# Optimization experiments

Measured on AMD Instinct MI355X. Metric: run time of the kernel, lower is better.

The kernel has to match this reference:

```python
import jax, jax.numpy as jnp
import numpy as np

N_NODES = 200000
N_EDGES = 3200000
N_GRAPHS = 64
IN_DIM, HIDDEN, OUT_DIM = 128, 16, 64


def setup_inputs() -> dict:
    key = jax.random.key(0)
    ks = jax.random.split(key, 5)
    x = jax.random.normal(ks[0], (N_NODES, IN_DIM), dtype=jnp.float32)
    edge_index = jax.random.randint(ks[1], (2, N_EDGES), 0, N_NODES, dtype=jnp.int64)
    batch = jnp.sort(jax.random.randint(ks[2], (N_NODES,), 0, N_GRAPHS, dtype=jnp.int64))
    W1 = jax.random.normal(ks[3], (IN_DIM, HIDDEN), dtype=jnp.float32) * (1.0 / np.sqrt(IN_DIM))
    W2 = jax.random.normal(ks[4], (HIDDEN, OUT_DIM), dtype=jnp.float32) * (1.0 / np.sqrt(HIDDEN))
    b1 = jnp.zeros((HIDDEN,), jnp.float32)
    b2 = jnp.zeros((OUT_DIM,), jnp.float32)
    return {"x": x, "edge_index": edge_index, "batch": batch,
            "W1": W1, "b1": b1, "W2": W2, "b2": b2, "training": 0}


def _gcn_conv(x, W, b, row, col, n_nodes):
    # PyG GCNConv: add-self-loop symmetric normalization, transform then
    # gather-from-row / scatter-add-to-col.  (row, col) already include self-loops.
    h = x @ W                                             # [N, out]
    deg = jnp.zeros((n_nodes,), h.dtype).at[col].add(1.0)  # degree incl. self-loop (>=1)
    dinv = deg ** -0.5
    norm = dinv[row] * dinv[col]                          # [E+N]
    out = jnp.zeros((n_nodes, W.shape[1]), h.dtype).at[col].add(h[row] * norm[:, None])
    return out + b


def reference(x, edge_index, batch, W1, b1, W2, b2, training):
    n = x.shape[0]
    loops = jnp.arange(n, dtype=edge_index.dtype)
    row = jnp.concatenate([edge_index[0], loops])
    col = jnp.concatenate([edge_index[1], loops])
    h = _gcn_conv(x, W1, b1, row, col, n)
    h = jax.nn.relu(h)
    # F.dropout with training=False is identity (reference is deterministic)
    h = _gcn_conv(h, W2, b2, row, col, n)
    # per-graph sum pooling: replaces the Python torch.where loop
    graph_embeds = jax.ops.segment_sum(h, batch, num_segments=N_GRAPHS)
    return graph_embeds
```

## Files before the change

kernel.cpp:

```cpp
#include <hip/hip_runtime.h>


#define TPB 256
#define CHUNK 4096
#define BK_SHIFT 9
#define NPB 512

__device__ __forceinline__ float bf2f(unsigned short u) {
    union { unsigned int i; float f; } v; v.i = ((unsigned int)u) << 16; return v.f;
}
__device__ __forceinline__ unsigned short f2bf(float f) {
    union { float f; unsigned int i; } v; v.f = f;
    unsigned int r = v.i + 0x7fff + ((v.i >> 16) & 1);
    return (unsigned short)(r >> 16);
}

__global__ __launch_bounds__(TPB) void hist_gemm_kernel(
        const int* __restrict__ col, int* __restrict__ counts,
        int E, int nblk, int nbuck,
        const float* __restrict__ x, const float* __restrict__ W1,
        unsigned short* __restrict__ h1b, int N, int nbg) {
    __shared__ int hist[NPB];
    __shared__ float w1s[128 * 16];
    int b = (int)blockIdx.x, t = threadIdx.x;
    int M = min(nblk, nbg);
    int role, id;
    if (b < 2 * M) { role = b & 1; id = b >> 1; }
    else           { role = (nblk > nbg) ? 0 : 1; id = b - M; }

    if (role == 0) {
        for (int i = t; i < nbuck; i += TPB) hist[i] = 0;
        __syncthreads();
        int e0 = id * CHUNK;
        for (int i = t; i < CHUNK; i += TPB) {
            int e = e0 + i;
            if (e < E) atomicAdd(&hist[col[e] >> BK_SHIFT], 1);
        }
        __syncthreads();
        for (int i = t; i < nbuck; i += TPB) counts[i * nblk + id] = hist[i];
        return;
    }
    for (int i = t; i < 128 * 16; i += TPB) w1s[i] = W1[i];
    __syncthreads();
    int n = id * TPB + t;
    if (n >= N) return;
    const float4* xr = (const float4*)(x + (size_t)n * 128);
    float acc[16];
#pragma unroll
    for (int k = 0; k < 16; ++k) acc[k] = 0.f;
#pragma unroll 1
    for (int g = 0; g < 8; ++g) {
        float4 v0 = xr[g * 4 + 0], v1 = xr[g * 4 + 1];
        float4 v2 = xr[g * 4 + 2], v3 = xr[g * 4 + 3];
        float xv[16] = {v0.x, v0.y, v0.z, v0.w, v1.x, v1.y, v1.z, v1.w,
                        v2.x, v2.y, v2.z, v2.w, v3.x, v3.y, v3.z, v3.w};
#pragma unroll
        for (int cc = 0; cc < 16; ++cc) {
            const float4* w4 = (const float4*)&w1s[(g * 16 + cc) * 16];
            float4 wa = w4[0], wb = w4[1], wc = w4[2], wd = w4[3];
            float xc = xv[cc];
            acc[0]  = fmaf(xc, wa.x, acc[0]);  acc[1]  = fmaf(xc, wa.y, acc[1]);
            acc[2]  = fmaf(xc, wa.z, acc[2]);  acc[3]  = fmaf(xc, wa.w, acc[3]);
            acc[4]  = fmaf(xc, wb.x, acc[4]);  acc[5]  = fmaf(xc, wb.y, acc[5]);
            acc[6]  = fmaf(xc, wb.z, acc[6]);  acc[7]  = fmaf(xc, wb.w, acc[7]);
            acc[8]  = fmaf(xc, wc.x, acc[8]);  acc[9]  = fmaf(xc, wc.y, acc[9]);
            acc[10] = fmaf(xc, wc.z, acc[10]); acc[11] = fmaf(xc, wc.w, acc[11]);
            acc[12] = fmaf(xc, wd.x, acc[12]); acc[13] = fmaf(xc, wd.y, acc[13]);
            acc[14] = fmaf(xc, wd.z, acc[14]); acc[15] = fmaf(xc, wd.w, acc[15]);
        }
    }
    unsigned int u[8];
#pragma unroll
    for (int j = 0; j < 8; ++j)
        u[j] = (unsigned int)f2bf(acc[2 * j]) | ((unsigned int)f2bf(acc[2 * j + 1]) << 16);
    uint4* o = (uint4*)(h1b + (size_t)n * 16);
    o[0] = make_uint4(u[0], u[1], u[2], u[3]);
    o[1] = make_uint4(u[4], u[5], u[6], u[7]);
}

__global__ __launch_bounds__(TPB) void scan1_kernel(const int* __restrict__ in,
                                                    int* __restrict__ out,
                                                    int* __restrict__ bsum, int L) {
    __shared__ int s[TPB];
    int t = threadIdx.x;
    int i = blockIdx.x * TPB + t;
    int d = (i < L) ? in[i] : 0;
    s[t] = d; __syncthreads();
    for (int off = 1; off < TPB; off <<= 1) {
        int v = (t >= off) ? s[t - off] : 0;
        __syncthreads();
        s[t] += v;
        __syncthreads();
    }
    if (i < L) out[i] = s[t] - d;
    if (t == TPB - 1) bsum[blockIdx.x] = s[t];
}

__global__ __launch_bounds__(1024) void scan2_kernel(int* __restrict__ bsum, int nb) {
    __shared__ int s[1024];
    int t = threadIdx.x;
    int i0 = t * 2, i1 = t * 2 + 1;
    int v0 = (i0 < nb) ? bsum[i0] : 0;
    int v1 = (i1 < nb) ? bsum[i1] : 0;
    int pv = v0 + v1;
    s[t] = pv; __syncthreads();
    for (int off = 1; off < 1024; off <<= 1) {
        int u = (t >= off) ? s[t - off] : 0;
        __syncthreads();
        s[t] += u;
        __syncthreads();
    }
    int exc = s[t] - pv;
    if (i0 < nb) bsum[i0] = exc;
    if (i1 < nb) bsum[i1] = exc + v0;
}

__device__ __forceinline__ int cbase_at(const int* counts, const int* bsum, int f) {
    return counts[f] + bsum[f >> 8];
}

__global__ __launch_bounds__(TPB) void scatter_kernel(
        const int* __restrict__ row, const int* __restrict__ col,
        const int* __restrict__ counts, const int* __restrict__ bsum,
        int E, int nblk, int nbuck, int* __restrict__ bucketed) {
    __shared__ int cur[NPB];
    int id = (int)blockIdx.x, t = threadIdx.x;
    for (int i = t; i < nbuck; i += TPB)
        cur[i] = cbase_at(counts, bsum, i * nblk + id);
    __syncthreads();
    int e0 = id * CHUNK;
    for (int i = t; i < CHUNK; i += TPB) {
        int e = e0 + i;
        if (e < E) {
            int c = col[e];
            int pos = atomicAdd(&cur[c >> BK_SHIFT], 1);
            bucketed[pos] = ((c & (NPB - 1)) << 18) | row[e];
        }
    }
}

__global__ __launch_bounds__(TPB) void sort_kernel(
        const int* __restrict__ bucketed,
        const int* __restrict__ counts, const int* __restrict__ bsum,
        int E, int nblk, int nbuck,
        int* __restrict__ csr, int* __restrict__ offs, float* __restrict__ dinv,
        const unsigned short* __restrict__ h1b, unsigned short* __restrict__ h1p, int N) {
    __shared__ int lhist[NPB];
    __shared__ int part[TPB];
    __shared__ float sdinv[NPB];
    int bk = blockIdx.x, t = threadIdx.x;
    int n0 = bk << BK_SHIFT;
    int n1 = min(n0 + NPB, N);
    int e0 = cbase_at(counts, bsum, bk * nblk);
    int e1 = (bk + 1 < nbuck) ? cbase_at(counts, bsum, (bk + 1) * nblk) : E;

    lhist[t] = 0; lhist[t + TPB] = 0;
    __syncthreads();
    for (int i = e0 + t; i < e1; i += TPB)
        atomicAdd(&lhist[bucketed[i] >> 18], 1);
    __syncthreads();

    int base = t * 2;
    int c0 = lhist[base], c1 = lhist[base + 1];
    int s = c0 + c1;
    part[t] = s;
    __syncthreads();
    for (int off = 1; off < TPB; off <<= 1) {
        int v = (t >= off) ? part[t - off] : 0;
        __syncthreads();
        part[t] += v;
        __syncthreads();
    }
    int o0 = e0 + part[t] - s;
    int o1 = o0 + c0;
    lhist[base] = o0; lhist[base + 1] = o1;
    sdinv[base]     = rsqrtf((float)c0 + 1.0f);
    sdinv[base + 1] = rsqrtf((float)c1 + 1.0f);
    int n = n0 + base;
    if (n + 0 < N) { offs[n + 0] = o0; dinv[n + 0] = sdinv[base]; }
    if (n + 1 < N) { offs[n + 1] = o1; dinv[n + 1] = sdinv[base + 1]; }
    __syncthreads();

    for (int i = e0 + t; i < e1; i += TPB) {
        int v = bucketed[i];
        int pos = atomicAdd(&lhist[v >> 18], 1);
        csr[pos] = v & 0x3FFFF;
    }
    int nq = (n1 - n0) * 4;
    for (int i = t; i < nq; i += TPB) {
        float dv = sdinv[i >> 2];
        uint2 u = ((const uint2*)h1b)[(size_t)n0 * 4 + i];
        float f0 = bf2f((unsigned short)(u.x & 0xffff));
        float f1 = bf2f((unsigned short)(u.x >> 16));
        float f2 = bf2f((unsigned short)(u.y & 0xffff));
        float f3 = bf2f((unsigned short)(u.y >> 16));
        ((ushort4*)h1p)[(size_t)n0 * 4 + i] =
            make_ushort4(f2bf(f0 * dv), f2bf(f1 * dv), f2bf(f2 * dv), f2bf(f3 * dv));
    }
    if (bk == 0 && t == 0) offs[N] = E;
}

__global__ __launch_bounds__(TPB) void gather1_kernel(const int* __restrict__ csr,
                                                      const int* __restrict__ offs,
                                                      const unsigned short* __restrict__ h1p,
                                                      const float* __restrict__ dinv,
                                                      const float* __restrict__ b1,
                                                      unsigned short* __restrict__ h2p, int N) {
    int t = threadIdx.x;
    int c = blockIdx.x * 16 + (t >> 4);
    int lane = t & 15;
    int half = lane >> 3;
    int kk = lane & 7;
    if (c >= N) return;
    int p0 = offs[c], p1 = offs[c + 1];
    float a0 = 0.f, a1 = 0.f;
    for (int p = p0; p < p1; p += 32) {
        int s_lo = csr[min(p + lane, p1 - 1)];
        int s_hi = csr[min(p + 16 + lane, p1 - 1)];
        int rem = p1 - p;
        unsigned int u[16];
#pragma unroll
        for (int j = 0; j < 8; ++j) {
            int sj = __shfl(s_lo, 2 * j + half, 16);
            u[j] = *(const unsigned int*)&h1p[(size_t)sj * 16 + 2 * kk];
        }
#pragma unroll
        for (int j = 8; j < 16; ++j) {
            int sj = __shfl(s_hi, 2 * j + half - 16, 16);
            u[j] = *(const unsigned int*)&h1p[(size_t)sj * 16 + 2 * kk];
        }
#pragma unroll
        for (int j = 0; j < 16; ++j) {
            bool ok = (2 * j + half) < rem;
            a0 += ok ? bf2f((unsigned short)(u[j] & 0xffff)) : 0.f;
            a1 += ok ? bf2f((unsigned short)(u[j] >> 16)) : 0.f;
        }
    }
    a0 += __shfl_xor(a0, 8, 16);
    a1 += __shfl_xor(a1, 8, 16);
    if (half == 0) {
        float dc = dinv[c];
        unsigned int us = *(const unsigned int*)&h1p[(size_t)c * 16 + 2 * kk];
        float s0 = bf2f((unsigned short)(us & 0xffff));
        float s1 = bf2f((unsigned short)(us >> 16));
        float r0 = fmaf(dc, a0 + s0, b1[2 * kk]);
        float r1 = fmaf(dc, a1 + s1, b1[2 * kk + 1]);
        r0 = dc * fmaxf(r0, 0.f);
        r1 = dc * fmaxf(r1, 0.f);
        unsigned int w = (unsigned int)f2bf(r0) | ((unsigned int)f2bf(r1) << 16);
        *(unsigned int*)&h2p[(size_t)c * 16 + 2 * kk] = w;
    }
}

__global__ __launch_bounds__(TPB) void gather2f_kernel(
        const int* __restrict__ csr, const int* __restrict__ offs,
        const unsigned short* __restrict__ h2p, const float* __restrict__ dinv,
        const float* __restrict__ W2, const float* __restrict__ b2,
        const int* __restrict__ batch, float* __restrict__ out, int N) {
    __shared__ float w2s[16 * 64];
    __shared__ float asT[64 * 17];
    __shared__ float pool[64];
    int t = threadIdx.x;
    for (int i = t; i < 16 * 64; i += TPB) w2s[i] = W2[i];
    if (t < 64) pool[t] = 0.f;

    int n0 = blockIdx.x * 64;
    int nLast = min(n0 + 63, N - 1);
    int g0 = batch[n0];
    bool uniform = (batch[nLast] == g0);

    int grp = t >> 4, lane = t & 15;
    int half = lane >> 3, kk = lane & 7;
#pragma unroll 1
    for (int it = 0; it < 4; ++it) {
        int m = grp * 4 + it;
        int c = n0 + m;
        if (c < N) {
            int p0 = offs[c], p1 = offs[c + 1];
            float a0 = 0.f, a1 = 0.f;
            for (int p = p0; p < p1; p += 32) {
                int s_lo = csr[min(p + lane, p1 - 1)];
                int s_hi = csr[min(p + 16 + lane, p1 - 1)];
                int rem = p1 - p;
                unsigned int u[16];
#pragma unroll
                for (int j = 0; j < 8; ++j) {
                    int sj = __shfl(s_lo, 2 * j + half, 16);
                    u[j] = *(const unsigned int*)&h2p[(size_t)sj * 16 + 2 * kk];
                }
#pragma unroll
                for (int j = 8; j < 16; ++j) {
                    int sj = __shfl(s_hi, 2 * j + half - 16, 16);
                    u[j] = *(const unsigned int*)&h2p[(size_t)sj * 16 + 2 * kk];
                }
#pragma unroll
                for (int j = 0; j < 16; ++j) {
                    bool ok = (2 * j + half) < rem;
                    a0 += ok ? bf2f((unsigned short)(u[j] & 0xffff)) : 0.f;
                    a1 += ok ? bf2f((unsigned short)(u[j] >> 16)) : 0.f;
                }
            }
            a0 += __shfl_xor(a0, 8, 16);
            a1 += __shfl_xor(a1, 8, 16);
            if (half == 0) {
                float dc = dinv[c];
                unsigned int us = *(const unsigned int*)&h2p[(size_t)c * 16 + 2 * kk];
                float s0 = bf2f((unsigned short)(us & 0xffff));
                float s1 = bf2f((unsigned short)(us >> 16));
                asT[m * 17 + 2 * kk]     = dc * (a0 + s0);
                asT[m * 17 + 2 * kk + 1] = dc * (a1 + s1);
            }
        }
    }
    __syncthreads();

    int wave = t >> 6, j = t & 63;
    float w2reg[16];
#pragma unroll
    for (int kx = 0; kx < 16; ++kx) w2reg[kx] = w2s[kx * 64 + j];
    float b2j = b2[j];
    float val = 0.f;
    int g_cur = -1;
#pragma unroll 1
    for (int mi = 0; mi < 16; ++mi) {
        int m = wave * 16 + mi;
        int c = n0 + m;
        if (c >= N) break;
        const float* ar = &asT[m * 17];
        float y = b2j;
#pragma unroll
        for (int kx = 0; kx < 16; ++kx) y = fmaf(ar[kx], w2reg[kx], y);
        if (uniform) {
            val += y;
        } else {
            int g = batch[c];
            if (g != g_cur) {
                if (g_cur >= 0) atomicAdd(&out[(size_t)g_cur * 64 + j], val);
                val = 0.f;
                g_cur = g;
            }
            val += y;
        }
    }
    if (uniform) {
        atomicAdd(&pool[j], val);
        __syncthreads();
        if (t < 64) atomicAdd(&out[(size_t)g0 * 64 + t], pool[t]);
    } else {
        if (g_cur >= 0) atomicAdd(&out[(size_t)g_cur * 64 + j], val);
    }
}

static inline size_t align64(size_t v) { return (v + 63) & ~(size_t)63; }

extern "C" void kernel_launch(void* const* d_in, const int* in_sizes, int n_in,
                              void* d_out, int out_size, void* d_ws, size_t ws_size,
                              hipStream_t stream) {
    const float* x     = (const float*)d_in[0];
    const int*   ei    = (const int*)d_in[1];
    const int*   batch = (const int*)d_in[2];
    const float* W1    = (const float*)d_in[3];
    const float* b1    = (const float*)d_in[4];
    const float* W2    = (const float*)d_in[5];
    const float* b2    = (const float*)d_in[6];

    const int N = in_sizes[0] / 128;
    const int E = in_sizes[1] / 2;
    const int* row = ei;
    const int* col = ei + E;

    const int NBLK  = (E + CHUNK - 1) / CHUNK;
    const int NBUCK = (N + NPB - 1) / NPB;
    const int L     = NBUCK * NBLK;
    const int NBS   = (L + TPB - 1) / TPB;
    const int NBG   = (N + TPB - 1) / TPB;

    char* p = (char*)d_ws;
    int*            counts   = (int*)p;            p += align64((size_t)L * 4);
    int*            bsum     = (int*)p;            p += align64(2048 * 4);
    int*            bucketed = (int*)p;            p += align64((size_t)E * 4);
    int*            csr      = (int*)p;            p += align64((size_t)E * 4);
    int*            offs     = (int*)p;            p += align64((size_t)(N + 1) * 4);
    float*          dinv     = (float*)p;          p += align64((size_t)N * 4);
    unsigned short* h1b      = (unsigned short*)p; p += align64((size_t)N * 16 * 2);
    unsigned short* h1p      = (unsigned short*)p; p += align64((size_t)N * 16 * 2);
    unsigned short* h2p      = (unsigned short*)p; p += align64((size_t)N * 16 * 2);
    float*          out      = (float*)d_out;

    hipMemsetAsync(out, 0, (size_t)out_size * sizeof(float), stream);

    hist_gemm_kernel<<<NBLK + NBG, TPB, 0, stream>>>(col, counts, E, NBLK, NBUCK,
                                                     x, W1, h1b, N, NBG);
    scan1_kernel<<<NBS, TPB, 0, stream>>>(counts, counts, bsum, L);
    scan2_kernel<<<1, 1024, 0, stream>>>(bsum, NBS);
    scatter_kernel<<<NBLK, TPB, 0, stream>>>(row, col, counts, bsum,
                                             E, NBLK, NBUCK, bucketed);
    sort_kernel<<<NBUCK, TPB, 0, stream>>>(bucketed, counts, bsum, E, NBLK, NBUCK,
                                           csr, offs, dinv, h1b, h1p, N);
    gather1_kernel<<<(N + 15) / 16, TPB, 0, stream>>>(csr, offs, h1p, dinv, b1, h2p, N);
    gather2f_kernel<<<(N + 63) / 64, TPB, 0, stream>>>(csr, offs, h2p, dinv,
                                                       W2, b2, batch, out, N);
}
```

Baseline: 378.5 us.

## Split the x@W1 GEMM across hist, scan1 and scatter kernels

The node-feature GEMM blocks (x@W1 to bf16), which used to run entirely inside the histogram kernel, are now spread over three launches: up to 128 blocks with the histogram, up to 128 with the first scan pass, and the rest with the scatter kernel. This puts the bandwidth-heavy GEMM alongside the small, latency-bound scan and the atomic-heavy scatter, so their idle hardware does GEMM work. Scan1 and scatter now need larger shared-memory footprints, which may lower occupancy. The scatter launch also grows by most of the GEMM blocks.

```diff
diff --git a/kernel.cpp b/kernel.cpp
--- a/kernel.cpp
+++ b/kernel.cpp
@@ -15,34 +15,19 @@
     return (unsigned short)(r >> 16);
 }
 
-__global__ __launch_bounds__(TPB) void hist_gemm_kernel(
-        const int* __restrict__ col, int* __restrict__ counts,
-        int E, int nblk, int nbuck,
-        const float* __restrict__ x, const float* __restrict__ W1,
-        unsigned short* __restrict__ h1b, int N, int nbg) {
-    __shared__ int hist[NPB];
-    __shared__ float w1s[128 * 16];
-    int b = (int)blockIdx.x, t = threadIdx.x;
-    int M = min(nblk, nbg);
-    int role, id;
-    if (b < 2 * M) { role = b & 1; id = b >> 1; }
-    else           { role = (nblk > nbg) ? 0 : 1; id = b - M; }
-
-    if (role == 0) {
-        for (int i = t; i < nbuck; i += TPB) hist[i] = 0;
-        __syncthreads();
-        int e0 = id * CHUNK;
-        for (int i = t; i < CHUNK; i += TPB) {
-            int e = e0 + i;
-            if (e < E) atomicAdd(&hist[col[e] >> BK_SHIFT], 1);
-        }
-        __syncthreads();
-        for (int i = t; i < nbuck; i += TPB) counts[i * nblk + id] = hist[i];
-        return;
-    }
+__device__ __forceinline__ int role_split(int b, int nPartner, int nGemm, int* id) {
+    int M = min(nPartner, nGemm);
+    if (b < 2 * M) { *id = b >> 1; return b & 1; }
+    *id = b - M;
+    return (nPartner > nGemm) ? 0 : 1;
+}
+
+__device__ __forceinline__ void gemm_role(int gid, int t, const float* __restrict__ x,
+                                          const float* __restrict__ W1, float* w1s,
+                                          unsigned short* __restrict__ h1b, int N) {
     for (int i = t; i < 128 * 16; i += TPB) w1s[i] = W1[i];
     __syncthreads();
-    int n = id * TPB + t;
+    int n = gid * TPB + t;
     if (n >= N) return;
     const float4* xr = (const float4*)(x + (size_t)n * 128);
     float acc[16];
@@ -78,22 +63,53 @@
     o[1] = make_uint4(u[4], u[5], u[6], u[7]);
 }
 
-__global__ __launch_bounds__(TPB) void scan1_kernel(const int* __restrict__ in,
-                                                    int* __restrict__ out,
-                                                    int* __restrict__ bsum, int L) {
+__global__ __launch_bounds__(TPB) void hist_gemm_kernel(
+        const int* __restrict__ col, int* __restrict__ counts,
+        int E, int nblk, int nbuck,
+        const float* __restrict__ x, const float* __restrict__ W1,
+        unsigned short* __restrict__ h1b, int N, int nGemm, int gemmBase) {
+    __shared__ int hist[NPB];
+    __shared__ float w1s[128 * 16];
+    int t = threadIdx.x, id;
+    int role = role_split((int)blockIdx.x, nblk, nGemm, &id);
+    if (role == 0) {
+        for (int i = t; i < nbuck; i += TPB) hist[i] = 0;
+        __syncthreads();
+        int e0 = id * CHUNK;
+        for (int i = t; i < CHUNK; i += TPB) {
+            int e = e0 + i;
+            if (e < E) atomicAdd(&hist[col[e] >> BK_SHIFT], 1);
+        }
+        __syncthreads();
+        for (int i = t; i < nbuck; i += TPB) counts[i * nblk + id] = hist[i];
+        return;
+    }
+    gemm_role(id + gemmBase, t, x, W1, w1s, h1b, N);
+}
+
+__global__ __launch_bounds__(TPB) void scan1_gemm_kernel(
+        int* __restrict__ counts, int* __restrict__ bsum, int L, int nScan,
+        const float* __restrict__ x, const float* __restrict__ W1,
+        unsigned short* __restrict__ h1b, int N, int nGemm, int gemmBase) {
+    __shared__ float w1s[128 * 16];
     __shared__ int s[TPB];
-    int t = threadIdx.x;
-    int i = blockIdx.x * TPB + t;
-    int d = (i < L) ? in[i] : 0;
-    s[t] = d; __syncthreads();
-    for (int off = 1; off < TPB; off <<= 1) {
-        int v = (t >= off) ? s[t - off] : 0;
-        __syncthreads();
-        s[t] += v;
-        __syncthreads();
-    }
-    if (i < L) out[i] = s[t] - d;
-    if (t == TPB - 1) bsum[blockIdx.x] = s[t];
+    int t = threadIdx.x, id;
+    int role = role_split((int)blockIdx.x, nScan, nGemm, &id);
+    if (role == 0) {
+        int i = id * TPB + t;
+        int d = (i < L) ? counts[i] : 0;
+        s[t] = d; __syncthreads();
+        for (int off = 1; off < TPB; off <<= 1) {
+            int v = (t >= off) ? s[t - off] : 0;
+            __syncthreads();
+            s[t] += v;
+            __syncthreads();
+        }
+        if (i < L) counts[i] = s[t] - d;
+        if (t == TPB - 1) bsum[id] = s[t];
+        return;
+    }
+    gemm_role(id + gemmBase, t, x, W1, w1s, h1b, N);
 }
 
 __global__ __launch_bounds__(1024) void scan2_kernel(int* __restrict__ bsum, int nb) {
@@ -119,24 +135,32 @@
     return counts[f] + bsum[f >> 8];
 }
 
-__global__ __launch_bounds__(TPB) void scatter_kernel(
+__global__ __launch_bounds__(TPB) void scatter_gemm_kernel(
         const int* __restrict__ row, const int* __restrict__ col,
         const int* __restrict__ counts, const int* __restrict__ bsum,
-        int E, int nblk, int nbuck, int* __restrict__ bucketed) {
+        int E, int nblk, int nbuck, int* __restrict__ bucketed,
+        const float* __restrict__ x, const float* __restrict__ W1,
+        unsigned short* __restrict__ h1b, int N, int nGemm, int gemmBase) {
     __shared__ int cur[NPB];
-    int id = (int)blockIdx.x, t = threadIdx.x;
-    for (int i = t; i < nbuck; i += TPB)
-        cur[i] = cbase_at(counts, bsum, i * nblk + id);
-    __syncthreads();
-    int e0 = id * CHUNK;
-    for (int i = t; i < CHUNK; i += TPB) {
-        int e = e0 + i;
-        if (e < E) {
-            int c = col[e];
-            int pos = atomicAdd(&cur[c >> BK_SHIFT], 1);
-            bucketed[pos] = ((c & (NPB - 1)) << 18) | row[e];
-        }
-    }
+    __shared__ float w1s[128 * 16];
+    int t = threadIdx.x, id;
+    int role = role_split((int)blockIdx.x, nblk, nGemm, &id);
+    if (role == 0) {
+        for (int i = t; i < nbuck; i += TPB)
+            cur[i] = cbase_at(counts, bsum, i * nblk + id);
+        __syncthreads();
+        int e0 = id * CHUNK;
+        for (int i = t; i < CHUNK; i += TPB) {
+            int e = e0 + i;
+            if (e < E) {
+                int c = col[e];
+                int pos = atomicAdd(&cur[c >> BK_SHIFT], 1);
+                bucketed[pos] = ((c & (NPB - 1)) << 18) | row[e];
+            }
+        }
+        return;
+    }
+    gemm_role(id + gemmBase, t, x, W1, w1s, h1b, N);
 }
 
 __global__ __launch_bounds__(TPB) void sort_kernel(
@@ -375,6 +399,10 @@
     const int NBS   = (L + TPB - 1) / TPB;
     const int NBG   = (N + TPB - 1) / TPB;
 
+    int NA = NBG < 128 ? NBG : 128;
+    int NB_ = (NBG - NA) < 128 ? (NBG - NA) : 128;
+    int NC = NBG - NA - NB_;
+
     char* p = (char*)d_ws;
     int*            counts   = (int*)p;            p += align64((size_t)L * 4);
     int*            bsum     = (int*)p;            p += align64(2048 * 4);
@@ -389,12 +417,14 @@
 
     hipMemsetAsync(out, 0, (size_t)out_size * sizeof(float), stream);
 
-    hist_gemm_kernel<<<NBLK + NBG, TPB, 0, stream>>>(col, counts, E, NBLK, NBUCK,
-                                                     x, W1, h1b, N, NBG);
-    scan1_kernel<<<NBS, TPB, 0, stream>>>(counts, counts, bsum, L);
+    hist_gemm_kernel<<<NBLK + NA, TPB, 0, stream>>>(col, counts, E, NBLK, NBUCK,
+                                                    x, W1, h1b, N, NA, 0);
+    scan1_gemm_kernel<<<NBS + NB_, TPB, 0, stream>>>(counts, bsum, L, NBS,
+                                                     x, W1, h1b, N, NB_, NA);
     scan2_kernel<<<1, 1024, 0, stream>>>(bsum, NBS);
-    scatter_kernel<<<NBLK, TPB, 0, stream>>>(row, col, counts, bsum,
-                                             E, NBLK, NBUCK, bucketed);
+    scatter_gemm_kernel<<<NBLK + NC, TPB, 0, stream>>>(row, col, counts, bsum,
+                                                       E, NBLK, NBUCK, bucketed,
+                                                       x, W1, h1b, N, NC, NA + NB_);
     sort_kernel<<<NBUCK, TPB, 0, stream>>>(bucketed, counts, bsum, E, NBLK, NBUCK,
                                            csr, offs, dinv, h1b, h1p, N);
     gather1_kernel<<<(N + 15) / 16, TPB, 0, stream>>>(csr, offs, h1p, dinv, b1, h2p, N);
```

Result: faster. 369.8 us (-2.3%).
